# Kernel tuning notes

Hardware: AMD Instinct MI355X
Metric: run time of the kernel (lower is better)

## Reference

```python
import jax, jax.numpy as jnp
import numpy as np

IN_CH, HID, OUT_CH, HEADS = 55, 128, 49, 4
D = HID * HEADS  # 512
N_NODES, N_EDGES = 20000, 320000
NEG_SLOPE = 0.2


def setup_inputs() -> dict:
    key = jax.random.key(0)
    ks = jax.random.split(key, 16)
    s = lambda *sh: 1.0 / np.sqrt(sh[0])
    x = jax.random.normal(ks[0], (N_NODES, IN_CH), dtype=jnp.float32)
    edge_index = jax.random.randint(ks[1], (2, N_EDGES), 0, N_NODES, dtype=jnp.int64)
    p = {
        'x': x,
        'edge_index': edge_index,
        # conv1 (GATv2: lin_l for source, lin_r for target, per-head att vector, out bias)
        'w1_l': jax.random.normal(ks[2], (IN_CH, D), jnp.float32) * s(IN_CH),
        'b1_l': jnp.zeros((D,), jnp.float32),
        'w1_r': jax.random.normal(ks[3], (IN_CH, D), jnp.float32) * s(IN_CH),
        'b1_r': jnp.zeros((D,), jnp.float32),
        'att1': jax.random.normal(ks[4], (HEADS, HID), jnp.float32) * s(HID),
        'bias1': jnp.zeros((D,), jnp.float32),
        # conv2
        'w2_l': jax.random.normal(ks[5], (D, D), jnp.float32) * s(D),
        'b2_l': jnp.zeros((D,), jnp.float32),
        'w2_r': jax.random.normal(ks[6], (D, D), jnp.float32) * s(D),
        'b2_r': jnp.zeros((D,), jnp.float32),
        'att2': jax.random.normal(ks[7], (HEADS, HID), jnp.float32) * s(HID),
        'bias2': jnp.zeros((D,), jnp.float32),
        # classifier
        'w_cls': jax.random.normal(ks[8], (D, OUT_CH), jnp.float32) * s(D),
        'b_cls': jnp.zeros((OUT_CH,), jnp.float32),
    }
    return p


def _gatv2(x, src, dst, n, wl, bl, wr, br, att, bias):
    # GATv2Conv, concat=True. messages flow src -> dst, softmax over dst neighborhoods.
    xl = (x @ wl + bl).reshape(n, HEADS, HID)  # source transform
    xr = (x @ wr + br).reshape(n, HEADS, HID)  # target transform
    e = jax.nn.leaky_relu(xl[src] + xr[dst], NEG_SLOPE)      # [E, H, C]
    score = jnp.einsum('ehc,hc->eh', e, att)                  # [E, H]
    m = jax.ops.segment_max(score, dst, num_segments=n)       # stable softmax per target
    alpha = jnp.exp(score - m[dst])
    denom = jax.ops.segment_sum(alpha, dst, num_segments=n)
    alpha = alpha / denom[dst]
    out = jax.ops.segment_sum(xl[src] * alpha[..., None], dst, num_segments=n)
    return out.reshape(n, D) + bias


def reference(x, edge_index, w1_l, b1_l, w1_r, b1_r, att1, bias1,
              w2_l, b2_l, w2_r, b2_r, att2, bias2, w_cls, b_cls):
    n = x.shape[0]
    # PyG GATv2Conv default add_self_loops=True
    loops = jnp.arange(n, dtype=edge_index.dtype)
    src = jnp.concatenate([edge_index[0], loops])
    dst = jnp.concatenate([edge_index[1], loops])
    h = _gatv2(x, src, dst, n, w1_l, b1_l, w1_r, b1_r, att1, bias1)
    h = jax.nn.elu(h)
    # dropout p=0.5 is identity at eval time
    h = _gatv2(h, src, dst, n, w2_l, b2_l, w2_r, b2_r, att2, bias2)
    h = jax.nn.elu(h)
    return h @ w_cls + b_cls
```

## Files before the change

### kernel.cpp

```cpp
#include <hip/hip_runtime.h>
#include <hip/hip_bf16.h>
#include <float.h>
#include <math.h>

#define N_NODES 20000
#define N_EDGES 320000
#define ET      (N_EDGES + N_NODES)
#define ETB     ((ET + 255) / 256)
#define NPB     ((N_NODES + 255) / 256)
#define DCH     512
#define D2      1024
#define INCH    55
#define INCHP   64
#define OUTCH   49
#define OUTCHP  128
#define NB      130

typedef _Float16 f16;
typedef _Float16 f16x2 __attribute__((ext_vector_type(2)));
typedef _Float16 f16x8 __attribute__((ext_vector_type(8)));
typedef float    f32x4 __attribute__((ext_vector_type(4)));

#define GPTR(p) ((const __attribute__((address_space(1))) void*)(p))
#define LPTR(p) ((__attribute__((address_space(3))) void*)(p))

__device__ __forceinline__ void transpose_tile(const float* __restrict__ w, f16* __restrict__ o,
                                               int K, int N, int Kp, int bx, int by, int t,
                                               f16 (*tile)[66]) {
    int k0 = by * 64, n0 = bx * 64;
    #pragma unroll
    for (int r = 0; r < 16; ++r) {
        int kl = (t >> 6) + r * 4, nl = t & 63;
        int gk = k0 + kl, gn = n0 + nl;
        tile[kl][nl] = (gk < K && gn < N) ? (f16)w[(size_t)gk * N + gn] : (f16)0.f;
    }
    __syncthreads();
    #pragma unroll
    for (int r = 0; r < 16; ++r) {
        int kl = t & 63, nl = (t >> 6) + r * 4;
        o[(size_t)(n0 + nl) * Kp + k0 + kl] = tile[kl][nl];
    }
}

__global__ __launch_bounds__(256) void prep_all(const float* __restrict__ x, f16* __restrict__ x_h,
                                                const float* __restrict__ w1l, const float* __restrict__ w1r,
                                                const float* __restrict__ w2l, const float* __restrict__ w2r,
                                                const float* __restrict__ wc,
                                                f16* __restrict__ w1T, f16* __restrict__ w2T,
                                                f16* __restrict__ wcT,
                                                int* __restrict__ zeroA,
                                                int* __restrict__ bcur) {
    __shared__ f16 tile[64][66];
    int b = blockIdx.x, t = threadIdx.x;
    if (b < 157) {
        int i = b * 256 + t;
        if (i < 40000) zeroA[i] = 0;
        else if (i < 40000 + NB) bcur[i - 40000] = 0;
        return;
    }
    b -= 157;
    if (b < 5000) {
        int i = b * 256 + t;
        int r = i >> 6, c = i & 63;
        x_h[i] = (c < INCH) ? (f16)x[r * INCH + c] : (f16)0.f;
        return;
    }
    b -= 5000;
    if (b < 8)  { transpose_tile(w1l, w1T, INCH, DCH, INCHP, b, 0, t, tile); return; }
    b -= 8;
    if (b < 8)  { transpose_tile(w1r, w1T + (size_t)DCH * INCHP, INCH, DCH, INCHP, b, 0, t, tile); return; }
    b -= 8;
    if (b < 64) { transpose_tile(w2l, w2T, DCH, DCH, DCH, b & 7, b >> 3, t, tile); return; }
    b -= 64;
    if (b < 64) { transpose_tile(w2r, w2T + (size_t)DCH * DCH, DCH, DCH, DCH, b & 7, b >> 3, t, tile); return; }
    b -= 64;
    transpose_tile(wc, wcT, DCH, OUTCH, DCH, b & 1, b >> 1, t, tile);
}

__global__ void count_kernel(const int* __restrict__ ei, int* __restrict__ counts) {
    int e = blockIdx.x * blockDim.x + threadIdx.x;
    if (e >= ET) return;
    int d = (e < N_EDGES) ? ei[N_EDGES + e] : (e - N_EDGES);
    atomicAdd(&counts[d], 1);
}

__global__ void scan_kernel(const int* __restrict__ counts, int* __restrict__ row_ptr,
                            int* __restrict__ bbase) {
    __shared__ int sdata[1024];
    __shared__ int bh[NB];
    int t = threadIdx.x;
    if (t < NB) bh[t] = 0;
    __syncthreads();
    int per = (N_NODES + 1023) / 1024;
    int b = t * per, e = min(N_NODES, b + per);
    int sum = 0;
    for (int i = b; i < e; ++i) {
        int c = counts[i];
        sum += c;
        atomicAdd(&bh[min(c, NB - 1)], 1);
    }
    sdata[t] = sum;
    __syncthreads();
    for (int off = 1; off < 1024; off <<= 1) {
        int v = (t >= off) ? sdata[t - off] : 0;
        __syncthreads();
        sdata[t] += v;
        __syncthreads();
    }
    int run = (t == 0) ? 0 : sdata[t - 1];
    if (t == 0) row_ptr[0] = 0;
    for (int i = b; i < e; ++i) { run += counts[i]; row_ptr[i + 1] = run; }
    __syncthreads();
    if (t == 0) {
        int acc = 0;
        for (int j = NB - 1; j >= 0; --j) { bbase[j] = acc; acc += bh[j]; }
    }
}

__global__ __launch_bounds__(256) void fill_perm_kernel(const int* __restrict__ ei,
                                                        const int* __restrict__ row_ptr,
                                                        const int* __restrict__ counts,
                                                        const int* __restrict__ bbase,
                                                        int* __restrict__ cursor,
                                                        int* __restrict__ bcur,
                                                        int* __restrict__ esrc,
                                                        int* __restrict__ perm) {
    int blk = blockIdx.x;
    if (blk < ETB) {
        int e = blk * 256 + threadIdx.x;
        if (e >= ET) return;
        int s, d;
        if (e < N_EDGES) { s = ei[e]; d = ei[N_EDGES + e]; }
        else             { s = d = e - N_EDGES; }
        int pos = row_ptr[d] + atomicAdd(&cursor[d], 1);
        esrc[pos] = s;
        return;
    }
    blk -= ETB;
    __shared__ int hist[NB], basep[NB];
    int t = threadIdx.x;
    for (int i = t; i < NB; i += 256) hist[i] = 0;
    __syncthreads();
    int n = blk * 256 + t;
    bool valid = n < N_NODES;
    int bkt = 0, rl = 0;
    if (valid) {
        bkt = min(counts[n], NB - 1);
        rl = atomicAdd(&hist[bkt], 1);
    }
    __syncthreads();
    for (int i = t; i < NB; i += 256)
        if (hist[i] > 0) basep[i] = atomicAdd(&bcur[i], hist[i]);
    __syncthreads();
    if (valid) perm[bbase[bkt] + basep[bkt] + rl] = n;
}

template<int OUT_F16, int DUAL>
__global__ __launch_bounds__(256) void gemm_f16(const f16* __restrict__ A,
                                                const f16* __restrict__ BT,
                                                const float* __restrict__ bl,
                                                const float* __restrict__ br,
                                                void* __restrict__ Cout,
                                                int M, int Ka, int Nv, int ldc) {
    __shared__ __align__(16) f16 As[128][64];
    __shared__ __align__(16) f16 Bs[128][64];
    const int tid = threadIdx.x;
    const int w = tid >> 6, lane = tid & 63;
    int nbx = gridDim.x;
    int nwg = nbx * gridDim.y;
    int bid = blockIdx.y * nbx + blockIdx.x;
    if ((nwg & 7) == 0) bid = (bid & 7) * (nwg >> 3) + (bid >> 3);
    const int m0 = (bid / nbx) * 128, n0 = (bid % nbx) * 128;
    const int wr = (w >> 1) * 64, wc = (w & 1) * 64;
    const int lrow = lane & 15, lk = lane >> 4;
    const int sw = lrow & 7;

    f32x4 acc[4][4] = {};

    for (int k0 = 0; k0 < Ka; k0 += 64) {
        #pragma unroll
        for (int i = 0; i < 4; ++i) {
            int idx = tid + 256 * i;
            int row = idx >> 3;
            int cg  = (idx & 7) ^ (row & 7);
            int gm = m0 + row; gm = gm < M ? gm : M - 1;
            const f16* gp = A + (size_t)gm * Ka + k0 + cg * 8;
            f16* lp = &As[0][0] + (size_t)(w * 64 + 256 * i) * 8;
            __builtin_amdgcn_global_load_lds(GPTR(gp), LPTR(lp), 16, 0, 0);
        }
        #pragma unroll
        for (int i = 0; i < 4; ++i) {
            int idx = tid + 256 * i;
            int row = idx >> 3;
            int cg  = (idx & 7) ^ (row & 7);
            const f16* gp = BT + (size_t)(n0 + row) * Ka + k0 + cg * 8;
            f16* lp = &Bs[0][0] + (size_t)(w * 64 + 256 * i) * 8;
            __builtin_amdgcn_global_load_lds(GPTR(gp), LPTR(lp), 16, 0, 0);
        }
        __syncthreads();
        #pragma unroll
        for (int kk = 0; kk < 64; kk += 32) {
            f16x8 af[4], bf[4];
            #pragma unroll
            for (int m = 0; m < 4; ++m)
                af[m] = *(const f16x8*)&As[wr + m * 16 + lrow][(((kk >> 3) + lk) ^ sw) * 8];
            #pragma unroll
            for (int n = 0; n < 4; ++n)
                bf[n] = *(const f16x8*)&Bs[wc + n * 16 + lrow][(((kk >> 3) + lk) ^ sw) * 8];
            #pragma unroll
            for (int m = 0; m < 4; ++m)
                #pragma unroll
                for (int n = 0; n < 4; ++n)
                    acc[m][n] = __builtin_amdgcn_mfma_f32_16x16x32_f16(af[m], bf[n], acc[m][n], 0, 0, 0);
        }
        __syncthreads();
    }

    const int orow = (lane >> 4) * 4, ocol = lane & 15;
    #pragma unroll
    for (int m = 0; m < 4; ++m) {
        #pragma unroll
        for (int r = 0; r < 4; ++r) {
            int gm = m0 + wr + m * 16 + orow + r;
            if (gm >= M) continue;
            #pragma unroll
            for (int n = 0; n < 4; ++n) {
                int gn = n0 + wc + n * 16 + ocol;
                if (gn >= Nv) continue;
                float bv = DUAL ? (gn < DCH ? bl[gn] : br[gn - DCH]) : bl[gn];
                float v = acc[m][n][r] + bv;
                if (OUT_F16) ((f16*)Cout)[(size_t)gm * ldc + gn] = (f16)v;
                else         ((float*)Cout)[(size_t)gm * ldc + gn] = v;
            }
        }
    }
}

#define PROC(cc0, cc1, pp)                                                      \
  {                                                                             \
    float sc0 = 0.f, sc1 = 0.f;                                                 \
    _Pragma("unroll")                                                           \
    for (int j = 0; j < 4; ++j) {                                               \
        f16x2 u0 = cc0.q[j] + xr0.q[j];                                         \
        f16x2 u1 = cc1.q[j] + xr1.q[j];                                         \
        f16x2 l0 = __builtin_elementwise_max(u0, u0 * k02);                     \
        f16x2 l1 = __builtin_elementwise_max(u1, u1 * k02);                     \
        sc0 = __builtin_amdgcn_fdot2(l0, at2[j], sc0, false);                   \
        sc1 = __builtin_amdgcn_fdot2(l1, at2[j], sc1, false);                   \
    }                                                                           \
    _Pragma("unroll")                                                           \
    for (int o = 8; o >= 1; o >>= 1) {                                          \
        sc0 += __shfl_xor(sc0, o, 64);                                          \
        sc1 += __shfl_xor(sc1, o, 64);                                          \
    }                                                                           \
    if ((pp) >= deg0) sc0 = -INFINITY;                                          \
    if ((pp) >= deg1) sc1 = -INFINITY;                                          \
    if (__any(sc0 > m0 + 8.f)) {                                                \
        float mn = fmaxf(m0, sc0); float f = __expf(m0 - mn);                   \
        d0 *= f;                                                                \
        _Pragma("unroll") for (int j = 0; j < 8; ++j) acc0[j] *= f;             \
        m0 = mn;                                                                \
    }                                                                           \
    float w0 = __expf(sc0 - m0); d0 += w0;                                      \
    _Pragma("unroll") for (int j = 0; j < 8; ++j) acc0[j] += w0 * (float)cc0.v[j]; \
    if (__any(sc1 > m1 + 8.f)) {                                                \
        float mn = fmaxf(m1, sc1); float f = __expf(m1 - mn);                   \
        d1 *= f;                                                                \
        _Pragma("unroll") for (int j = 0; j < 8; ++j) acc1[j] *= f;             \
        m1 = mn;                                                                \
    }                                                                           \
    float w1 = __expf(sc1 - m1); d1 += w1;                                      \
    _Pragma("unroll") for (int j = 0; j < 8; ++j) acc1[j] += w1 * (float)cc1.v[j]; \
  }

__global__ __launch_bounds__(256) void edge_agg6(const int* __restrict__ row_ptr,
                                                 const int* __restrict__ esrc,
                                                 const int* __restrict__ perm,
                                                 const f16* __restrict__ xlr,
                                                 const float* __restrict__ att,
                                                 const float* __restrict__ bias,
                                                 f16* __restrict__ out) {
    int wv = (blockIdx.x * 256 + threadIdx.x) >> 6;
    if (wv * 2 >= N_NODES) return;
    int n0 = perm[wv * 2], n1 = perm[wv * 2 + 1];
    int lane = threadIdx.x & 63;

    union U8 { f16x8 v; f16x2 q[4]; };
    U8 xr0, xr1;
    xr0.v = *(const f16x8*)(xlr + (size_t)n0 * D2 + DCH + lane * 8);
    xr1.v = *(const f16x8*)(xlr + (size_t)n1 * D2 + DCH + lane * 8);
    const float4* av = (const float4*)(att + lane * 8);
    float4 a0 = av[0], a1 = av[1];
    f16x2 at2[4] = { f16x2{(f16)a0.x, (f16)a0.y}, f16x2{(f16)a0.z, (f16)a0.w},
                     f16x2{(f16)a1.x, (f16)a1.y}, f16x2{(f16)a1.z, (f16)a1.w} };
    const f16x2 k02 = {(f16)0.2f, (f16)0.2f};

    int beg0 = row_ptr[n0], deg0 = row_ptr[n0 + 1] - beg0;
    int beg1 = row_ptr[n1], deg1 = row_ptr[n1 + 1] - beg1;
    int pre0 = (lane < deg0) ? esrc[beg0 + lane] : 0;
    int pre1 = (lane < deg1) ? esrc[beg1 + lane] : 0;

    float acc0[8] = {}, acc1[8] = {};
    float m0 = -FLT_MAX, m1 = -FLT_MAX, d0 = 0.f, d1 = 0.f;

    int dmax = deg0 > deg1 ? deg0 : deg1;
    int dcap = dmax < 64 ? dmax : 64;

    U8 cA0, cA1, cB0, cB1;
    {
        int s0 = __shfl(pre0, 0, 64), s1 = __shfl(pre1, 0, 64);
        cA0.v = *(const f16x8*)(xlr + (size_t)s0 * D2 + lane * 8);
        cA1.v = *(const f16x8*)(xlr + (size_t)s1 * D2 + lane * 8);
    }
    int p = 0;
    for (; p + 1 < dcap; p += 2) {
        int t0 = __shfl(pre0, p + 1, 64), t1 = __shfl(pre1, p + 1, 64);
        cB0.v = *(const f16x8*)(xlr + (size_t)t0 * D2 + lane * 8);
        cB1.v = *(const f16x8*)(xlr + (size_t)t1 * D2 + lane * 8);
        PROC(cA0, cA1, p)
        if (p + 2 < dcap) {
            int u0 = __shfl(pre0, p + 2, 64), u1 = __shfl(pre1, p + 2, 64);
            cA0.v = *(const f16x8*)(xlr + (size_t)u0 * D2 + lane * 8);
            cA1.v = *(const f16x8*)(xlr + (size_t)u1 * D2 + lane * 8);
        }
        PROC(cB0, cB1, p + 1)
    }
    if (p < dcap) PROC(cA0, cA1, p)
    for (p = 64; p < dmax; ++p) {
        int s0 = (p < deg0) ? esrc[beg0 + p] : -1;
        int s1 = (p < deg1) ? esrc[beg1 + p] : -1;
        U8 t0, t1;
        t0.v = *(const f16x8*)(xlr + (size_t)(s0 < 0 ? 0 : s0) * D2 + lane * 8);
        t1.v = *(const f16x8*)(xlr + (size_t)(s1 < 0 ? 0 : s1) * D2 + lane * 8);
        PROC(t0, t1, p)
    }

    const float4* bv = (const float4*)(bias + lane * 8);
    float4 b0 = bv[0], b1 = bv[1];
    float bf[8] = {b0.x, b0.y, b0.z, b0.w, b1.x, b1.y, b1.z, b1.w};
    float i0 = 1.f / d0, i1 = 1.f / d1;
    f16x8 o0, o1;
    #pragma unroll
    for (int j = 0; j < 8; ++j) {
        float v0 = acc0[j] * i0 + bf[j];
        float v1 = acc1[j] * i1 + bf[j];
        v0 = v0 > 0.f ? v0 : __expf(v0) - 1.f;
        v1 = v1 > 0.f ? v1 : __expf(v1) - 1.f;
        o0[j] = (f16)v0;
        o1[j] = (f16)v1;
    }
    *(f16x8*)(out + (size_t)n0 * DCH + lane * 8) = o0;
    *(f16x8*)(out + (size_t)n1 * DCH + lane * 8) = o1;
}

extern "C" void kernel_launch(void* const* d_in, const int* in_sizes, int n_in,
                              void* d_out, int out_size, void* d_ws, size_t ws_size,
                              hipStream_t stream) {
    const float* x     = (const float*)d_in[0];
    const int*   ei    = (const int*)d_in[1];
    const float* w1_l  = (const float*)d_in[2];
    const float* b1_l  = (const float*)d_in[3];
    const float* w1_r  = (const float*)d_in[4];
    const float* b1_r  = (const float*)d_in[5];
    const float* att1  = (const float*)d_in[6];
    const float* bias1 = (const float*)d_in[7];
    const float* w2_l  = (const float*)d_in[8];
    const float* b2_l  = (const float*)d_in[9];
    const float* w2_r  = (const float*)d_in[10];
    const float* b2_r  = (const float*)d_in[11];
    const float* att2  = (const float*)d_in[12];
    const float* bias2 = (const float*)d_in[13];
    const float* wcls  = (const float*)d_in[14];
    const float* bcls  = (const float*)d_in[15];
    float* out = (float*)d_out;

    char* ws = (char*)d_ws;
    f16* x_h = (f16*)ws;
    f16* w1T = x_h + (size_t)N_NODES * INCHP;
    f16* w2T = w1T + (size_t)D2 * INCHP;
    f16* wcT = w2T + (size_t)D2 * DCH;
    f16* xlr = wcT + (size_t)OUTCHP * DCH;
    f16* h   = xlr + (size_t)N_NODES * D2;
    int* row_ptr = (int*)(h + (size_t)N_NODES * DCH);
    int* counts  = row_ptr + (N_NODES + 1);
    int* cursor  = counts + N_NODES;
    int* esrc    = cursor + N_NODES;
    int* perm    = esrc + ET;
    int* bbase   = perm + N_NODES;
    int* bcur    = bbase + NB;

    prep_all<<<5317, 256, 0, stream>>>(x, x_h, w1_l, w1_r, w2_l, w2_r, wcls,
                                       w1T, w2T, wcT, counts, bcur);
    count_kernel<<<(ET + 255) / 256, 256, 0, stream>>>(ei, counts);
    scan_kernel<<<1, 1024, 0, stream>>>(counts, row_ptr, bbase);
    fill_perm_kernel<<<ETB + NPB, 256, 0, stream>>>(ei, row_ptr, counts, bbase,
                                                    cursor, bcur, esrc, perm);

    dim3 blk(256);
    dim3 gD(D2 / 128, (N_NODES + 127) / 128);
    dim3 gC(1, (N_NODES + 127) / 128);
    int eb = (N_NODES / 2 + 3) / 4;

    gemm_f16<1, 1><<<gD, blk, 0, stream>>>(x_h, w1T, b1_l, b1_r, xlr, N_NODES, INCHP, D2, D2);
    edge_agg6<<<eb, blk, 0, stream>>>(row_ptr, esrc, perm, xlr, att1, bias1, h);
    gemm_f16<1, 1><<<gD, blk, 0, stream>>>(h, w2T, b2_l, b2_r, xlr, N_NODES, DCH, D2, D2);
    edge_agg6<<<eb, blk, 0, stream>>>(row_ptr, esrc, perm, xlr, att2, bias2, h);
    gemm_f16<0, 0><<<gC, blk, 0, stream>>>(h, wcT, bcls, bcls, out, N_NODES, DCH, OUTCH, OUTCH);
}
```

Baseline: 273.7 us.

## Use fp16 packed accumulation, triple-buffer neighbor loads, vectorize GEMM epilogue

The GEMM now swaps its MFMA operands so each lane holds four consecutive output columns, which lets the fp16 epilogue write f16x4 vectors with a float4 bias load instead of scalar stores. In the edge aggregation kernel the per-node accumulators move from fp32 to packed fp16, using f16x2 multiply-add to halve the VALU work. The online-softmax rescale threshold is lowered from 8 to 2 to keep fp16 values in range. Neighbor row loads become a three-deep rotating buffer to hide more gather latency. The fp16 accumulation risks lower accuracy on high-degree nodes.

Result: faster. 255.3 us (-6.7%).

```diff
diff --git a/kernel.cpp b/kernel.cpp
--- a/kernel.cpp
+++ b/kernel.cpp
@@ -18,6 +18,7 @@
 
 typedef _Float16 f16;
 typedef _Float16 f16x2 __attribute__((ext_vector_type(2)));
+typedef _Float16 f16x4 __attribute__((ext_vector_type(4)));
 typedef _Float16 f16x8 __attribute__((ext_vector_type(8)));
 typedef float    f32x4 __attribute__((ext_vector_type(4)));
 
@@ -211,26 +212,38 @@
             for (int m = 0; m < 4; ++m)
                 #pragma unroll
                 for (int n = 0; n < 4; ++n)
-                    acc[m][n] = __builtin_amdgcn_mfma_f32_16x16x32_f16(af[m], bf[n], acc[m][n], 0, 0, 0);
+                    acc[m][n] = __builtin_amdgcn_mfma_f32_16x16x32_f16(bf[n], af[m], acc[m][n], 0, 0, 0);
         }
         __syncthreads();
     }
 
-    const int orow = (lane >> 4) * 4, ocol = lane & 15;
+    const int om = lane & 15, on4 = (lane >> 4) * 4;
     #pragma unroll
-    for (int m = 0; m < 4; ++m) {
-        #pragma unroll
-        for (int r = 0; r < 4; ++r) {
-            int gm = m0 + wr + m * 16 + orow + r;
-            if (gm >= M) continue;
+    for (int nn = 0; nn < 4; ++nn) {
+        int gn0 = n0 + wc + nn * 16 + on4;
+        if (OUT_F16) {
+            const float* bp = (DUAL && gn0 >= DCH) ? (br + gn0 - DCH) : (bl + gn0);
+            float4 bv = *(const float4*)bp;
+            float bfr[4] = {bv.x, bv.y, bv.z, bv.w};
             #pragma unroll
-            for (int n = 0; n < 4; ++n) {
-                int gn = n0 + wc + n * 16 + ocol;
-                if (gn >= Nv) continue;
-                float bv = DUAL ? (gn < DCH ? bl[gn] : br[gn - DCH]) : bl[gn];
-                float v = acc[m][n][r] + bv;
-                if (OUT_F16) ((f16*)Cout)[(size_t)gm * ldc + gn] = (f16)v;
-                else         ((float*)Cout)[(size_t)gm * ldc + gn] = v;
+            for (int mm = 0; mm < 4; ++mm) {
+                int gm = m0 + wr + mm * 16 + om;
+                if (gm >= M) continue;
+                f16x4 o;
+                #pragma unroll
+                for (int r = 0; r < 4; ++r) o[r] = (f16)(acc[mm][nn][r] + bfr[r]);
+                *(f16x4*)((f16*)Cout + (size_t)gm * ldc + gn0) = o;
+            }
+        } else {
+            #pragma unroll
+            for (int mm = 0; mm < 4; ++mm) {
+                int gm = m0 + wr + mm * 16 + om;
+                if (gm >= M) continue;
+                #pragma unroll
+                for (int r = 0; r < 4; ++r) {
+                    int gn = gn0 + r;
+                    if (gn < Nv) ((float*)Cout)[(size_t)gm * ldc + gn] = acc[mm][nn][r] + bl[gn];
+                }
             }
         }
     }
@@ -255,25 +268,41 @@
     }                                                                           \
     if ((pp) >= deg0) sc0 = -INFINITY;                                          \
     if ((pp) >= deg1) sc1 = -INFINITY;                                          \
-    if (__any(sc0 > m0 + 8.f)) {                                                \
-        float mn = fmaxf(m0, sc0); float f = __expf(m0 - mn);                   \
-        d0 *= f;                                                                \
-        _Pragma("unroll") for (int j = 0; j < 8; ++j) acc0[j] *= f;             \
+    if (__any(sc0 > m0 + 2.f)) {                                                \
+        float mn = fmaxf(m0, sc0);                                              \
+        f16 fh = (f16)__expf(m0 - mn);                                          \
+        f16x2 fh2 = {fh, fh};                                                   \
+        d0 *= (float)fh;                                                        \
+        _Pragma("unroll") for (int j = 0; j < 4; ++j) acc0.q[j] *= fh2;         \
         m0 = mn;                                                                \
     }                                                                           \
-    float w0 = __expf(sc0 - m0); d0 += w0;                                      \
-    _Pragma("unroll") for (int j = 0; j < 8; ++j) acc0[j] += w0 * (float)cc0.v[j]; \
-    if (__any(sc1 > m1 + 8.f)) {                                                \
-        float mn = fmaxf(m1, sc1); float f = __expf(m1 - mn);                   \
-        d1 *= f;                                                                \
-        _Pragma("unroll") for (int j = 0; j < 8; ++j) acc1[j] *= f;             \
+    { f16 wh = (f16)__expf(sc0 - m0); d0 += (float)wh;                          \
+      f16x2 wh2 = {wh, wh};                                                     \
+      _Pragma("unroll") for (int j = 0; j < 4; ++j)                             \
+          acc0.q[j] += wh2 * cc0.q[j]; }                                        \
+    if (__any(sc1 > m1 + 2.f)) {                                                \
+        float mn = fmaxf(m1, sc1);                                              \
+        f16 fh = (f16)__expf(m1 - mn);                                          \
+        f16x2 fh2 = {fh, fh};                                                   \
+        d1 *= (float)fh;                                                        \
+        _Pragma("unroll") for (int j = 0; j < 4; ++j) acc1.q[j] *= fh2;         \
         m1 = mn;                                                                \
     }                                                                           \
-    float w1 = __expf(sc1 - m1); d1 += w1;                                      \
-    _Pragma("unroll") for (int j = 0; j < 8; ++j) acc1[j] += w1 * (float)cc1.v[j]; \
+    { f16 wh = (f16)__expf(sc1 - m1); d1 += (float)wh;                          \
+      f16x2 wh2 = {wh, wh};                                                     \
+      _Pragma("unroll") for (int j = 0; j < 4; ++j)                             \
+          acc1.q[j] += wh2 * cc1.q[j]; }                                        \
   }
 
-__global__ __launch_bounds__(256) void edge_agg6(const int* __restrict__ row_ptr,
+#define LOADU(B0, B1, pp)                                                       \
+  {                                                                             \
+    int q = (pp) < dcap ? (pp) : dcap - 1;                                      \
+    int s0 = __shfl(pre0, q, 64), s1 = __shfl(pre1, q, 64);                     \
+    B0.v = *(const f16x8*)(xlr + (size_t)s0 * D2 + lane * 8);                   \
+    B1.v = *(const f16x8*)(xlr + (size_t)s1 * D2 + lane * 8);                   \
+  }
+
+__global__ __launch_bounds__(256) void edge_agg9(const int* __restrict__ row_ptr,
                                                  const int* __restrict__ esrc,
                                                  const int* __restrict__ perm,
                                                  const f16* __restrict__ xlr,
@@ -300,38 +329,33 @@
     int pre0 = (lane < deg0) ? esrc[beg0 + lane] : 0;
     int pre1 = (lane < deg1) ? esrc[beg1 + lane] : 0;
 
-    float acc0[8] = {}, acc1[8] = {};
+    U8 acc0, acc1;
+    acc0.v = (f16x8)(f16)0.f;
+    acc1.v = (f16x8)(f16)0.f;
     float m0 = -FLT_MAX, m1 = -FLT_MAX, d0 = 0.f, d1 = 0.f;
 
     int dmax = deg0 > deg1 ? deg0 : deg1;
     int dcap = dmax < 64 ? dmax : 64;
 
-    U8 cA0, cA1, cB0, cB1;
-    {
-        int s0 = __shfl(pre0, 0, 64), s1 = __shfl(pre1, 0, 64);
-        cA0.v = *(const f16x8*)(xlr + (size_t)s0 * D2 + lane * 8);
-        cA1.v = *(const f16x8*)(xlr + (size_t)s1 * D2 + lane * 8);
-    }
-    int p = 0;
-    for (; p + 1 < dcap; p += 2) {
-        int t0 = __shfl(pre0, p + 1, 64), t1 = __shfl(pre1, p + 1, 64);
-        cB0.v = *(const f16x8*)(xlr + (size_t)t0 * D2 + lane * 8);
-        cB1.v = *(const f16x8*)(xlr + (size_t)t1 * D2 + lane * 8);
+    U8 cA0, cA1, cB0, cB1, cC0, cC1;
+    LOADU(cA0, cA1, 0)
+    LOADU(cB0, cB1, 1)
+    for (int p = 0; p < dcap; p += 3) {
+        LOADU(cC0, cC1, p + 2)
         PROC(cA0, cA1, p)
-        if (p + 2 < dcap) {
-            int u0 = __shfl(pre0, p + 2, 64), u1 = __shfl(pre1, p + 2, 64);
-            cA0.v = *(const f16x8*)(xlr + (size_t)u0 * D2 + lane * 8);
-            cA1.v = *(const f16x8*)(xlr + (size_t)u1 * D2 + lane * 8);
-        }
+        if (p + 1 >= dcap) break;
+        LOADU(cA0, cA1, p + 3)
         PROC(cB0, cB1, p + 1)
-    }
-    if (p < dcap) PROC(cA0, cA1, p)
-    for (p = 64; p < dmax; ++p) {
-        int s0 = (p < deg0) ? esrc[beg0 + p] : -1;
-        int s1 = (p < deg1) ? esrc[beg1 + p] : -1;
+        if (p + 2 >= dcap) break;
+        LOADU(cB0, cB1, p + 4)
+        PROC(cC0, cC1, p + 2)
+    }
+    for (int p = 64; p < dmax; ++p) {
+        int s0 = (p < deg0) ? esrc[beg0 + p] : 0;
+        int s1 = (p < deg1) ? esrc[beg1 + p] : 0;
         U8 t0, t1;
-        t0.v = *(const f16x8*)(xlr + (size_t)(s0 < 0 ? 0 : s0) * D2 + lane * 8);
-        t1.v = *(const f16x8*)(xlr + (size_t)(s1 < 0 ? 0 : s1) * D2 + lane * 8);
+        t0.v = *(const f16x8*)(xlr + (size_t)s0 * D2 + lane * 8);
+        t1.v = *(const f16x8*)(xlr + (size_t)s1 * D2 + lane * 8);
         PROC(t0, t1, p)
     }
 
@@ -342,8 +366,8 @@
     f16x8 o0, o1;
     #pragma unroll
     for (int j = 0; j < 8; ++j) {
-        float v0 = acc0[j] * i0 + bf[j];
-        float v1 = acc1[j] * i1 + bf[j];
+        float v0 = (float)acc0.v[j] * i0 + bf[j];
+        float v1 = (float)acc1.v[j] * i1 + bf[j];
         v0 = v0 > 0.f ? v0 : __expf(v0) - 1.f;
         v1 = v1 > 0.f ? v1 : __expf(v1) - 1.f;
         o0[j] = (f16)v0;
@@ -402,8 +426,8 @@
     int eb = (N_NODES / 2 + 3) / 4;
 
     gemm_f16<1, 1><<<gD, blk, 0, stream>>>(x_h, w1T, b1_l, b1_r, xlr, N_NODES, INCHP, D2, D2);
-    edge_agg6<<<eb, blk, 0, stream>>>(row_ptr, esrc, perm, xlr, att1, bias1, h);
+    edge_agg9<<<eb, blk, 0, stream>>>(row_ptr, esrc, perm, xlr, att1, bias1, h);
     gemm_f16<1, 1><<<gD, blk, 0, stream>>>(h, w2T, b2_l, b2_r, xlr, N_NODES, DCH, D2, D2);
-    edge_agg6<<<eb, blk, 0, stream>>>(row_ptr, esrc, perm, xlr, att2, bias2, h);
+    edge_agg9<<<eb, blk, 0, stream>>>(row_ptr, esrc, perm, xlr, att2, bias2, h);
     gemm_f16<0, 0><<<gC, blk, 0, stream>>>(h, wcT, bcls, bcls, out, N_NODES, DCH, OUTCH, OUTCH);
 }
```
